# Optimization experiments

Hardware: AMD Instinct MI355X
Metric: run time of the kernel (lower is better)

Reference implementation:

```python
import jax, jax.numpy as jnp
import numpy as np

N = 50000      # nodes
E = 400000     # edges (avg degree 8)
C = 128        # dim_single (node_dim)
DP = 64        # dim_pair (edge_dim)
HID = 256      # dim_egnn_hidden
DEPTH = 4      # depth_equivariant
M_IN = 2 * C + DP  # node_mlp / coord_mlp input dim = 320


def setup_inputs() -> dict:
    key = jax.random.key(0)
    ks = jax.random.split(key, 12)
    def w(k, shape, fan):
        return jax.random.normal(k, shape, jnp.float32) / np.float32(np.sqrt(fan))
    return {
        'single': jax.random.normal(ks[0], (N, C), jnp.float32),
        'pair': jax.random.normal(ks[1], (1,), jnp.float32),  # unused (se3t/ipa disabled)
        'coords': jax.random.normal(ks[2], (N, 3), jnp.float32),
        'edge_index': jax.random.randint(ks[3], (2, E), 0, N, jnp.int32),
        'edge_dist': jax.random.uniform(ks[4], (E,), jnp.float32),
        # stacked per-layer EGNN params (leading DEPTH axis, consumed by lax.scan)
        'We1': w(ks[5], (DEPTH, 1, DP), 1), 'be1': jnp.zeros((DEPTH, DP), jnp.float32),
        'We2': w(ks[6], (DEPTH, DP, DP), DP), 'be2': jnp.zeros((DEPTH, DP), jnp.float32),
        'Wn1': w(ks[7], (DEPTH, M_IN, HID), M_IN), 'bn1': jnp.zeros((DEPTH, HID), jnp.float32),
        'Wn2': w(ks[8], (DEPTH, HID, C), HID), 'bn2': jnp.zeros((DEPTH, C), jnp.float32),
        'Wc1': w(ks[9], (DEPTH, M_IN, HID), M_IN), 'bc1': jnp.zeros((DEPTH, HID), jnp.float32),
        'Wc2': w(ks[10], (DEPTH, HID, 1), HID),  # coord_mlp final layer has no bias
        'gamma': jnp.ones((C,), jnp.float32), 'beta': jnp.zeros((C,), jnp.float32),
    }


def _egnn_stack(h, x, edge_index, edge_dist, params):
    src, dst = edge_index[0], edge_index[1]
    n_nodes = h.shape[0]
    def layer(carry, p):
        h, x = carry
        We1, be1, We2, be2, Wn1, bn1, Wn2, bn2, Wc1, bc1, Wc2 = p
        # edge_mlp(edge_dist)
        ea = jax.nn.silu(edge_dist[:, None] @ We1 + be1) @ We2 + be2        # [E, DP]
        # gather -> concat -> MLP (message)
        mi = jnp.concatenate([h[src], h[dst], ea], axis=-1)                 # [E, 2C+DP]
        m = jax.nn.silu(mi @ Wn1 + bn1) @ Wn2 + bn2                         # [E, C]
        h = h + jax.ops.segment_sum(m, dst, num_segments=n_nodes)          # index_add on dst
        # coordinate update
        cw = jax.nn.silu(mi @ Wc1 + bc1) @ Wc2                              # [E, 1]
        x = x + jax.ops.segment_sum(cw * (x[src] - x[dst]), dst, num_segments=n_nodes)
        return (h, x), None
    (h, x), _ = jax.lax.scan(layer, (h, x), params)
    return h, x


def reference(single, pair, coords, edge_index, edge_dist,
              We1, be1, We2, be2, Wn1, bn1, Wn2, bn2, Wc1, bc1, Wc2,
              gamma, beta):
    h, x = _egnn_stack(single, coords, edge_index, edge_dist,
                       (We1, be1, We2, be2, Wn1, bn1, Wn2, bn2, Wc1, bc1, Wc2))
    # final LayerNorm (eps=1e-5, matching nn.LayerNorm default)
    mu = h.mean(-1, keepdims=True)
    var = ((h - mu) ** 2).mean(-1, keepdims=True)
    out = gamma * (h - mu) * jax.lax.rsqrt(var + 1e-5) + beta
    return out, x
```

## Files before the change

kernel.cpp:

```cpp
#include <hip/hip_runtime.h>
#include <hip/hip_bf16.h>
#include <math.h>

#define NN 50000
#define NE 400000
#define CD 128
#define EPB 64
#define HBINS 50176

typedef __attribute__((ext_vector_type(8))) short bf16x8;
typedef __attribute__((ext_vector_type(4))) float f32x4;

__device__ __forceinline__ float silu_f(float z) {
    return z * __builtin_amdgcn_rcpf(1.f + __expf(-z));
}
__device__ __forceinline__ unsigned short f2bf(float x) {
    unsigned int u = __float_as_uint(x);
    u = (u + 0x7FFFu + ((u >> 16) & 1u)) >> 16;
    return (unsigned short)u;
}
__device__ __forceinline__ unsigned pk_bf16(float a, float b) {
    union { __hip_bfloat162 h2; unsigned u; } cv;
    cv.h2 = __float22bfloat162_rn(make_float2(a, b));
    return cv.u;
}

__global__ __launch_bounds__(256) void hist_kernel(
        const int* __restrict__ dst, int* __restrict__ hist)
{
    int e = blockIdx.x * 256 + threadIdx.x;
    if (e < NE) atomicAdd(&hist[dst[e]], 1);
}

__global__ __launch_bounds__(256) void scan1_kernel(
        const int* __restrict__ hist, int* __restrict__ offs, int* __restrict__ bsum)
{
    __shared__ int sh[256];
    const int t = threadIdx.x;
    const int i = blockIdx.x * 256 + t;
    int v = hist[i];
    sh[t] = v;
    __syncthreads();
    for (int off = 1; off < 256; off <<= 1) {
        int x = (t >= off) ? sh[t - off] : 0;
        __syncthreads();
        sh[t] += x;
        __syncthreads();
    }
    offs[i] = sh[t] - v;
    if (t == 255) bsum[blockIdx.x] = sh[t];
}

__global__ __launch_bounds__(256) void scan2_kernel(int* __restrict__ bsum)
{
    __shared__ int sh[256];
    const int t = threadIdx.x;
    int v = (t < 196) ? bsum[t] : 0;
    sh[t] = v;
    __syncthreads();
    for (int off = 1; off < 256; off <<= 1) {
        int x = (t >= off) ? sh[t - off] : 0;
        __syncthreads();
        sh[t] += x;
        __syncthreads();
    }
    if (t < 196) bsum[t] = sh[t] - v;
}

__global__ __launch_bounds__(256) void scan3_kernel(
        const int* __restrict__ offs, const int* __restrict__ bsum,
        int* __restrict__ cursor)
{
    const int i = blockIdx.x * 256 + threadIdx.x;
    cursor[i] = offs[i] + bsum[blockIdx.x];
}

__global__ __launch_bounds__(256) void scatter_kernel(
        const int* __restrict__ eidx, const float* __restrict__ edist,
        int* __restrict__ cursor,
        int* __restrict__ ssrc, int* __restrict__ sdst, float* __restrict__ sdist)
{
    int e = blockIdx.x * 256 + threadIdx.x;
    if (e < NE) {
        int d = eidx[NE + e];
        int p = atomicAdd(&cursor[d], 1);
        ssrc[p] = eidx[e];
        sdst[p] = d;
        sdist[p] = edist[e];
    }
}

__global__ __launch_bounds__(64) void wbig_prep(
        const float* __restrict__ We2, const float* __restrict__ Wn1,
        const float* __restrict__ Wc1, unsigned short* __restrict__ wbig)
{
    const int l = blockIdx.y;
    const int ntile = blockIdx.x / 10;
    const int ks = blockIdx.x % 10;
    const int lane = threadIdx.x;
    const int n = ntile * 16 + (lane & 15);
    const int kbase = ks * 32 + (lane >> 4) * 8;
    const float* Wn1l = Wn1 + (size_t)l * 320 * 256;
    const float* Wc1l = Wc1 + (size_t)l * 320 * 256;
    const float* We2l = We2 + (size_t)l * 64 * 64;
    const float* W1 = (n < 256) ? Wn1l : Wc1l;
    const int nn = n & 255;
    unsigned short* outp = wbig + ((((size_t)l * 32 + ntile) * 10 + ks) * 64 + lane) * 8;
    #pragma unroll
    for (int j = 0; j < 8; ++j) {
        int k = kbase + j;
        float val;
        if (k < 256) {
            val = W1[(size_t)k * 256 + nn];
        } else {
            int i = k - 256;
            float acc = 0.f;
            #pragma unroll 8
            for (int jj = 0; jj < 64; ++jj)
                acc += We2l[i * 64 + jj] * W1[(size_t)(256 + jj) * 256 + nn];
            val = acc;
        }
        outp[j] = f2bf(val);
    }
}

__global__ __launch_bounds__(64) void wn2_prep(
        const float* __restrict__ Wn2, unsigned short* __restrict__ wn2s)
{
    const int l = blockIdx.y;
    const int ntile = blockIdx.x / 8;
    const int ks = blockIdx.x % 8;
    const int lane = threadIdx.x;
    const int n = ntile * 16 + (lane & 15);
    const int kbase = ks * 32 + (lane >> 4) * 8;
    const float* Wn2l = Wn2 + (size_t)l * 256 * 128;
    unsigned short* outp = wn2s + ((((size_t)l * 8 + ntile) * 8 + ks) * 64 + lane) * 8;
    #pragma unroll
    for (int j = 0; j < 8; ++j)
        outp[j] = f2bf(Wn2l[(size_t)(kbase + j) * 128 + n]);
}

__global__ __launch_bounds__(512) void cep_prep(
        const float* __restrict__ be2,
        const float* __restrict__ Wn1, const float* __restrict__ Wc1,
        const float* __restrict__ bn1, const float* __restrict__ bc1,
        float* __restrict__ cep)
{
    const int l = blockIdx.x;
    const int j = threadIdx.x;
    const int jj = j & 255;
    const float* W1 = ((j < 256) ? Wn1 : Wc1) + (size_t)l * 320 * 256;
    const float* be2l = be2 + l * 64;
    float acc = (j < 256) ? bn1[l * 256 + jj] : bc1[l * 256 + jj];
    #pragma unroll 8
    for (int k = 0; k < 64; ++k)
        acc += be2l[k] * W1[(size_t)(256 + k) * 256 + jj];
    cep[l * 512 + j] = acc;
}

__global__ __launch_bounds__(256) void conv_kernel(
        const float* __restrict__ h, unsigned short* __restrict__ hbf)
{
    const int i = (blockIdx.x * 256 + threadIdx.x) * 4;
    float4 v = *(const float4*)(h + i);
    *(uint2*)(hbf + i) = make_uint2(pk_bf16(v.x, v.y), pk_bf16(v.z, v.w));
}

__global__ __launch_bounds__(512, 4) void edge_kernel(
        const int* __restrict__ ssrc, const int* __restrict__ sdst,
        const float* __restrict__ sdist,
        const float* __restrict__ We1l, const float* __restrict__ be1l,
        const unsigned short* __restrict__ hbf,
        const unsigned short* __restrict__ wbig_l,
        const float* __restrict__ cep_l,
        const float* __restrict__ Wc2l,
        const float* __restrict__ x_in,
        float* __restrict__ Tbar, float* __restrict__ x_out)
{
    __shared__ __align__(16) unsigned short s_A[EPB][328];
    __shared__ __align__(16) unsigned short s_tT[256][72];
    __shared__ __align__(16) float s_cw[EPB][4];
    __shared__ __align__(16) unsigned short s_rid[EPB];
    __shared__ int s_src[EPB], s_dst[EPB];
    __shared__ int s_rdst[EPB];
    __shared__ unsigned long long s_mask;

    const int tid = threadIdx.x;
    const int eb = blockIdx.x * EPB;

    if (tid < EPB) {
        int dv = sdst[eb + tid];
        s_src[tid] = ssrc[eb + tid];
        s_dst[tid] = dv;
        int nxt = (tid == EPB - 1) ? -1 : sdst[eb + tid + 1];
        unsigned long long mk = __ballot(dv != nxt);
        int rid = __popcll(mk & ((1ull << tid) - 1ull));
        s_rid[tid] = (unsigned short)rid;
        if (dv != nxt) s_rdst[rid] = dv;
        if (tid == 0) s_mask = mk;
    }
    {
        const int e = tid >> 3;
        const int j0 = (tid & 7) * 8;
        const float d = sdist[eb + e];
        unsigned tmp[4];
        #pragma unroll
        for (int j = 0; j < 4; ++j) {
            float a = silu_f(d * We1l[j0 + 2 * j] + be1l[j0 + 2 * j]);
            float b = silu_f(d * We1l[j0 + 2 * j + 1] + be1l[j0 + 2 * j + 1]);
            tmp[j] = pk_bf16(a, b);
        }
        *(bf16x8*)&s_A[e][j0 + 256] = *(const bf16x8*)tmp;
    }
    __syncthreads();

    #pragma unroll
    for (int it = 0; it < 4; ++it) {
        const int c = tid + it * 512;
        const int row = c >> 5, ch = c & 31;
        const int node = (ch < 16) ? s_src[row] : s_dst[row];
        const int koff = (ch & 15) * 8;
        bf16x8 v = *(const bf16x8*)(hbf + (size_t)node * CD + koff);
        *(bf16x8*)&s_A[row][ch * 8] = v;
    }
    __syncthreads();

    const int wave = tid >> 6, lane = tid & 63;
    const int m = lane & 15, q = lane >> 4;

    f32x4 acc[4][4];
    #pragma unroll
    for (int nt = 0; nt < 4; ++nt)
        #pragma unroll
        for (int mt = 0; mt < 4; ++mt)
            acc[nt][mt] = (f32x4){0.f, 0.f, 0.f, 0.f};

    __builtin_amdgcn_s_setprio(1);
    if (wave < 4) {
        #pragma unroll
        for (int ks = 0; ks < 10; ++ks) {
            const int koff = ks * 32 + q * 8;
            bf16x8 ef[4];
            #pragma unroll
            for (int mt = 0; mt < 4; ++mt)
                ef[mt] = *(const bf16x8*)&s_A[mt * 16 + m][koff];
            #pragma unroll
            for (int nt = 0; nt < 4; ++nt) {
                bf16x8 wf = *(const bf16x8*)(wbig_l +
                    ((size_t)((wave * 4 + nt) * 10 + ks) * 64 + lane) * 8);
                #pragma unroll
                for (int mt = 0; mt < 4; ++mt)
                    acc[nt][mt] = __builtin_amdgcn_mfma_f32_16x16x32_bf16(
                        ef[mt], wf, acc[nt][mt], 0, 0, 0);
            }
        }
    } else {
        #pragma unroll
        for (int ks = 0; ks < 10; ++ks) {
            const int koff = ks * 32 + q * 8;
            bf16x8 ef[4];
            #pragma unroll
            for (int mt = 0; mt < 4; ++mt)
                ef[mt] = *(const bf16x8*)&s_A[mt * 16 + m][koff];
            #pragma unroll
            for (int nt = 0; nt < 4; ++nt) {
                bf16x8 wf = *(const bf16x8*)(wbig_l +
                    ((size_t)((wave * 4 + nt) * 10 + ks) * 64 + lane) * 8);
                #pragma unroll
                for (int mt = 0; mt < 4; ++mt)
                    acc[nt][mt] = __builtin_amdgcn_mfma_f32_16x16x32_bf16(
                        wf, ef[mt], acc[nt][mt], 0, 0, 0);
            }
        }
    }
    __builtin_amdgcn_s_setprio(0);

    if (wave < 4) {
        #pragma unroll
        for (int nt = 0; nt < 4; ++nt) {
            const int col = (wave * 4 + nt) * 16 + m;
            const float ce = cep_l[col];
            #pragma unroll
            for (int mt = 0; mt < 4; ++mt) {
                float t0 = silu_f(acc[nt][mt][0] + ce);
                float t1 = silu_f(acc[nt][mt][1] + ce);
                float t2 = silu_f(acc[nt][mt][2] + ce);
                float t3 = silu_f(acc[nt][mt][3] + ce);
                *(uint2*)&s_tT[col][(mt * 16 + q * 4) ^ ((m & 3) << 3)] =
                    make_uint2(pk_bf16(t0, t1), pk_bf16(t2, t3));
            }
        }
    } else {
        float p[4] = {0.f, 0.f, 0.f, 0.f};
        #pragma unroll
        for (int nt = 0; nt < 4; ++nt) {
            const int c0 = (wave * 4 + nt) * 16 + q * 4;
            const float4 ce = *(const float4*)&cep_l[c0];
            const float4 wv = *(const float4*)&Wc2l[c0 - 256];
            #pragma unroll
            for (int mt = 0; mt < 4; ++mt) {
                p[mt] += silu_f(acc[nt][mt][0] + ce.x) * wv.x;
                p[mt] += silu_f(acc[nt][mt][1] + ce.y) * wv.y;
                p[mt] += silu_f(acc[nt][mt][2] + ce.z) * wv.z;
                p[mt] += silu_f(acc[nt][mt][3] + ce.w) * wv.w;
            }
        }
        #pragma unroll
        for (int mt = 0; mt < 4; ++mt) {
            p[mt] += __shfl_xor(p[mt], 16);
            p[mt] += __shfl_xor(p[mt], 32);
        }
        if (lane < 16) {
            #pragma unroll
            for (int mt = 0; mt < 4; ++mt)
                s_cw[mt * 16 + lane][wave - 4] = p[mt];
        }
    }
    __syncthreads();

    {
        const unsigned long long mask = s_mask;
        const int nruns = __popcll(mask);
        f32x4 a2[2][4];
        #pragma unroll
        for (int mt2 = 0; mt2 < 2; ++mt2)
            #pragma unroll
            for (int nt = 0; nt < 4; ++nt)
                a2[mt2][nt] = (f32x4){0.f, 0.f, 0.f, 0.f};
        #pragma unroll
        for (int ks = 0; ks < 2; ++ks) {
            bf16x8 af[2];
            #pragma unroll
            for (int mt2 = 0; mt2 < 2; ++mt2)
                af[mt2] = *(const bf16x8*)&s_tT[(wave * 2 + mt2) * 16 + m]
                                           [(ks * 32 + q * 8) ^ ((m & 3) << 3)];
            const unsigned* rp = (const unsigned*)&s_rid[ks * 32 + q * 8];
            const unsigned r01 = rp[0], r23 = rp[1], r45 = rp[2], r67 = rp[3];
            #pragma unroll
            for (int nt = 0; nt < 4; ++nt) {
                const unsigned n = (unsigned)(nt * 16 + m);
                unsigned gw[4];
                gw[0] = ((r01 & 0xFFFFu) == n ? 0x3F80u : 0u) |
                        ((r01 >> 16)      == n ? 0x3F800000u : 0u);
                gw[1] = ((r23 & 0xFFFFu) == n ? 0x3F80u : 0u) |
                        ((r23 >> 16)      == n ? 0x3F800000u : 0u);
                gw[2] = ((r45 & 0xFFFFu) == n ? 0x3F80u : 0u) |
                        ((r45 >> 16)      == n ? 0x3F800000u : 0u);
                gw[3] = ((r67 & 0xFFFFu) == n ? 0x3F80u : 0u) |
                        ((r67 >> 16)      == n ? 0x3F800000u : 0u);
                const bf16x8 bfr = *(const bf16x8*)gw;
                #pragma unroll
                for (int mt2 = 0; mt2 < 2; ++mt2)
                    a2[mt2][nt] = __builtin_amdgcn_mfma_f32_16x16x32_bf16(
                        af[mt2], bfr, a2[mt2][nt], 0, 0, 0);
            }
        }
        #pragma unroll
        for (int nt = 0; nt < 4; ++nt) {
            const int r = nt * 16 + m;
            if (r < nruns) {
                float* bp = Tbar + (size_t)s_rdst[r] * 256;
                const bool bdry = (r == 0) || (r == nruns - 1);
                #pragma unroll
                for (int mt2 = 0; mt2 < 2; ++mt2) {
                    const int c = (wave * 2 + mt2) * 16 + q * 4;
                    if (bdry) {
                        atomicAdd(&bp[c],     a2[mt2][nt][0]);
                        atomicAdd(&bp[c + 1], a2[mt2][nt][1]);
                        atomicAdd(&bp[c + 2], a2[mt2][nt][2]);
                        atomicAdd(&bp[c + 3], a2[mt2][nt][3]);
                    } else {
                        *(f32x4*)&bp[c] = a2[mt2][nt];
                    }
                }
            }
        }
    }
    if (wave == 2) {
        const int e = lane;
        float4 pv = *(const float4*)&s_cw[e][0];
        float cw = pv.x + pv.y + pv.z + pv.w;
        int sn = s_src[e], dn = s_dst[e];
        float dx0 = x_in[sn * 3 + 0] - x_in[dn * 3 + 0];
        float dx1 = x_in[sn * 3 + 1] - x_in[dn * 3 + 1];
        float dx2 = x_in[sn * 3 + 2] - x_in[dn * 3 + 2];
        atomicAdd(&x_out[dn * 3 + 0], cw * dx0);
        atomicAdd(&x_out[dn * 3 + 1], cw * dx1);
        atomicAdd(&x_out[dn * 3 + 2], cw * dx2);
    }
}

__global__ __launch_bounds__(256) void node_kernel(
        const float* __restrict__ Tbar, const int* __restrict__ deg,
        const unsigned short* __restrict__ wn2_l, const float* __restrict__ bn2l,
        float* __restrict__ h, unsigned short* __restrict__ hbf)
{
    const int nb = blockIdx.x * 64;
    const int tid = threadIdx.x;
    const int wave = tid >> 6, lane = tid & 63;
    const int m = lane & 15, q = lane >> 4;

    f32x4 acc[2][4];
    #pragma unroll
    for (int nt = 0; nt < 2; ++nt)
        #pragma unroll
        for (int mt = 0; mt < 4; ++mt)
            acc[nt][mt] = (f32x4){0.f, 0.f, 0.f, 0.f};

    #pragma unroll
    for (int ks = 0; ks < 8; ++ks) {
        bf16x8 af[4];
        #pragma unroll
        for (int mt = 0; mt < 4; ++mt) {
            const int node = nb + mt * 16 + m;
            if (node < NN) {
                const float* tp = Tbar + (size_t)node * 256 + ks * 32 + q * 8;
                float4 f0 = *(const float4*)tp;
                float4 f1 = *(const float4*)(tp + 4);
                unsigned u[4] = { pk_bf16(f0.x, f0.y), pk_bf16(f0.z, f0.w),
                                  pk_bf16(f1.x, f1.y), pk_bf16(f1.z, f1.w) };
                af[mt] = *(const bf16x8*)u;
            } else {
                af[mt] = (bf16x8){0,0,0,0,0,0,0,0};
            }
        }
        #pragma unroll
        for (int nt = 0; nt < 2; ++nt) {
            bf16x8 wf = *(const bf16x8*)(wn2_l +
                ((size_t)((wave * 2 + nt) * 8 + ks) * 64 + lane) * 8);
            #pragma unroll
            for (int mt = 0; mt < 4; ++mt)
                acc[nt][mt] = __builtin_amdgcn_mfma_f32_16x16x32_bf16(af[mt], wf, acc[nt][mt], 0, 0, 0);
        }
    }

    {
        float* tz = (float*)Tbar;
        #pragma unroll
        for (int ks = 0; ks < 8; ++ks) {
            #pragma unroll
            for (int mt = 0; mt < 4; ++mt) {
                const int node = nb + mt * 16 + m;
                if (node < NN && wave == (ks & 3)) {
                    float* tp = tz + (size_t)node * 256 + ks * 32 + q * 8;
                    *(f32x4*)tp       = (f32x4){0.f, 0.f, 0.f, 0.f};
                    *(f32x4*)(tp + 4) = (f32x4){0.f, 0.f, 0.f, 0.f};
                }
            }
        }
    }

    #pragma unroll
    for (int nt = 0; nt < 2; ++nt) {
        const int col = (wave * 2 + nt) * 16 + m;
        const float bb = bn2l[col];
        #pragma unroll
        for (int mt = 0; mt < 4; ++mt) {
            #pragma unroll
            for (int i = 0; i < 4; ++i) {
                const int node = nb + mt * 16 + q * 4 + i;
                if (node < NN) {
                    float val = acc[nt][mt][i] + (float)deg[node] * bb
                              + h[(size_t)node * CD + col];
                    h[(size_t)node * CD + col] = val;
                    hbf[(size_t)node * CD + col] = f2bf(val);
                }
            }
        }
    }
}

__global__ __launch_bounds__(256) void final_kernel(
        const float* __restrict__ h, const float* __restrict__ x,
        const float* __restrict__ gamma, const float* __restrict__ beta,
        float* __restrict__ out)
{
    const int lane = threadIdx.x & 63;
    const int wave = threadIdx.x >> 6;
    const int n = blockIdx.x * 4 + wave;
    float v0 = h[(size_t)n * CD + lane];
    float v1 = h[(size_t)n * CD + 64 + lane];
    float ssum = v0 + v1;
    for (int off = 32; off; off >>= 1) ssum += __shfl_xor(ssum, off);
    float mu = ssum * (1.f / 128.f);
    float d0 = v0 - mu, d1 = v1 - mu;
    float sq = d0 * d0 + d1 * d1;
    for (int off = 32; off; off >>= 1) sq += __shfl_xor(sq, off);
    float rstd = rsqrtf(sq * (1.f / 128.f) + 1e-5f);
    out[(size_t)n * CD + lane]      = gamma[lane]      * d0 * rstd + beta[lane];
    out[(size_t)n * CD + 64 + lane] = gamma[64 + lane] * d1 * rstd + beta[64 + lane];
    if (threadIdx.x < 12) {
        int nn = blockIdx.x * 4 + threadIdx.x / 3;
        int c = threadIdx.x % 3;
        out[(size_t)NN * CD + nn * 3 + c] = x[nn * 3 + c];
    }
}

static inline size_t align_up(size_t v) { return (v + 255) & ~(size_t)255; }

extern "C" void kernel_launch(void* const* d_in, const int* in_sizes, int n_in,
                              void* d_out, int out_size, void* d_ws, size_t ws_size,
                              hipStream_t stream)
{
    const float* single = (const float*)d_in[0];
    const float* coords = (const float*)d_in[2];
    const int*   eidx   = (const int*)d_in[3];
    const float* edist  = (const float*)d_in[4];
    const float* We1 = (const float*)d_in[5];
    const float* be1 = (const float*)d_in[6];
    const float* We2 = (const float*)d_in[7];
    const float* be2 = (const float*)d_in[8];
    const float* Wn1 = (const float*)d_in[9];
    const float* bn1 = (const float*)d_in[10];
    const float* Wn2 = (const float*)d_in[11];
    const float* bn2 = (const float*)d_in[12];
    const float* Wc1 = (const float*)d_in[13];
    const float* bc1 = (const float*)d_in[14];
    const float* Wc2 = (const float*)d_in[15];
    const float* gamma = (const float*)d_in[16];
    const float* beta  = (const float*)d_in[17];
    float* out = (float*)d_out;

    char* w = (char*)d_ws;
    float* h0  = (float*)w;  w += align_up((size_t)NN * CD * 4);
    float* x0  = (float*)w;  w += align_up((size_t)NN * 3 * 4);
    float* x1  = (float*)w;  w += align_up((size_t)NN * 3 * 4);
    unsigned short* hbf  = (unsigned short*)w; w += align_up((size_t)NN * CD * 2);
    unsigned short* wbig = (unsigned short*)w; w += align_up((size_t)4 * 512 * 320 * 2);
    unsigned short* wn2s = (unsigned short*)w; w += align_up((size_t)4 * 256 * 128 * 2);
    float* cep = (float*)w;  w += align_up((size_t)4 * 512 * 4);
    int* hist   = (int*)w;   w += align_up((size_t)HBINS * 4);
    int* offs   = (int*)w;   w += align_up((size_t)HBINS * 4);
    int* cursor = (int*)w;   w += align_up((size_t)HBINS * 4);
    int* bsum   = (int*)w;   w += align_up((size_t)256 * 4);
    int* ssrc   = (int*)w;   w += align_up((size_t)NE * 4);
    int* sdst   = (int*)w;   w += align_up((size_t)NE * 4);
    float* sdist = (float*)w; w += align_up((size_t)NE * 4);
    float* Tbar = (float*)w; w += align_up((size_t)NN * 256 * 4);

    hipMemsetAsync(hist, 0, (size_t)HBINS * 4, stream);
    hist_kernel<<<(NE + 255) / 256, 256, 0, stream>>>(eidx + NE, hist);
    scan1_kernel<<<HBINS / 256, 256, 0, stream>>>(hist, offs, bsum);
    scan2_kernel<<<1, 256, 0, stream>>>(bsum);
    scan3_kernel<<<HBINS / 256, 256, 0, stream>>>(offs, bsum, cursor);
    scatter_kernel<<<(NE + 255) / 256, 256, 0, stream>>>(eidx, edist, cursor, ssrc, sdst, sdist);

    wbig_prep<<<dim3(320, 4), 64, 0, stream>>>(We2, Wn1, Wc1, wbig);
    wn2_prep<<<dim3(64, 4), 64, 0, stream>>>(Wn2, wn2s);
    cep_prep<<<4, 512, 0, stream>>>(be2, Wn1, Wc1, bn1, bc1, cep);

    hipMemcpyAsync(h0, single, (size_t)NN * CD * 4, hipMemcpyDeviceToDevice, stream);
    hipMemcpyAsync(x0, coords, (size_t)NN * 3 * 4, hipMemcpyDeviceToDevice, stream);
    conv_kernel<<<(NN * CD) / 1024, 256, 0, stream>>>(single, hbf);

    hipMemsetAsync(Tbar, 0, (size_t)NN * 256 * 4, stream);

    float* xc = x0; float* xn = x1;
    for (int l = 0; l < 4; ++l) {
        hipMemcpyAsync(xn, xc, (size_t)NN * 3 * 4, hipMemcpyDeviceToDevice, stream);
        edge_kernel<<<NE / EPB, 512, 0, stream>>>(
            ssrc, sdst, sdist,
            We1 + l * 64, be1 + l * 64,
            hbf,
            wbig + (size_t)l * 512 * 320,
            cep + l * 512,
            Wc2 + l * 256,
            xc, Tbar, xn);
        node_kernel<<<(NN + 63) / 64, 256, 0, stream>>>(
            Tbar, hist,
            wn2s + (size_t)l * 256 * 128,
            bn2 + l * CD, h0, hbf);
        float* t = xc; xc = xn; xn = t;
    }
    final_kernel<<<NN / 4, 256, 0, stream>>>(h0, xc, gamma, beta, out);
}
```

Before: 1.410 ms.

## Store interior per-node aggregates in bf16, keep fp32 atomics only for boundary nodes

The edge kernel writes aggregated per-node hidden activations for runs fully inside a block as bf16 into a separate buffer. Runs on block boundaries still use fp32 atomics into a side buffer. A per-node flag tells the node kernel which buffer to read. This halves traffic for most aggregate writes and reads, and replaces the zeroing loop in the node kernel with a bf16 memset plus a small zeroing kernel that clears only boundary rows. It also drops the setprio hints around the MFMA loops. Nodes with no edges read the memset zero bf16 buffer. The cost is extra launches per layer and a flag lookup in the node kernel.

```diff
diff --git a/kernel.cpp b/kernel.cpp
--- a/kernel.cpp
+++ b/kernel.cpp
@@ -6,6 +6,7 @@
 #define NE 400000
 #define CD 128
 #define EPB 64
+#define NBLK (NE / EPB)
 #define HBINS 50176
 
 typedef __attribute__((ext_vector_type(8))) short bf16x8;
@@ -88,6 +89,26 @@
         sdst[p] = d;
         sdist[p] = edist[e];
     }
+}
+
+__global__ __launch_bounds__(256) void bflag_kernel(
+        const int* __restrict__ sdst, unsigned char* __restrict__ bflag)
+{
+    int b = blockIdx.x * 256 + threadIdx.x;
+    if (b < NBLK) {
+        bflag[sdst[b * EPB]] = 1;
+        bflag[sdst[b * EPB + EPB - 1]] = 1;
+    }
+}
+
+__global__ __launch_bounds__(128) void zside_kernel(
+        const int* __restrict__ sdst, float* __restrict__ Tf32)
+{
+    const int b = blockIdx.x;
+    const int t = threadIdx.x;
+    const int r = (t < 64) ? sdst[b * EPB] : sdst[b * EPB + EPB - 1];
+    *(float4*)(Tf32 + (size_t)r * 256 + (t & 63) * 4) =
+        make_float4(0.f, 0.f, 0.f, 0.f);
 }
 
 __global__ __launch_bounds__(64) void wbig_prep(
@@ -175,7 +196,8 @@
         const float* __restrict__ cep_l,
         const float* __restrict__ Wc2l,
         const float* __restrict__ x_in,
-        float* __restrict__ Tbar, float* __restrict__ x_out)
+        unsigned short* __restrict__ Tbf, float* __restrict__ Tf32,
+        float* __restrict__ x_out)
 {
     __shared__ __align__(16) unsigned short s_A[EPB][328];
     __shared__ __align__(16) unsigned short s_tT[256][72];
@@ -235,7 +257,6 @@
         for (int mt = 0; mt < 4; ++mt)
             acc[nt][mt] = (f32x4){0.f, 0.f, 0.f, 0.f};
 
-    __builtin_amdgcn_s_setprio(1);
     if (wave < 4) {
         #pragma unroll
         for (int ks = 0; ks < 10; ++ks) {
@@ -273,7 +294,6 @@
             }
         }
     }
-    __builtin_amdgcn_s_setprio(0);
 
     if (wave < 4) {
         #pragma unroll
@@ -359,18 +379,25 @@
         for (int nt = 0; nt < 4; ++nt) {
             const int r = nt * 16 + m;
             if (r < nruns) {
-                float* bp = Tbar + (size_t)s_rdst[r] * 256;
                 const bool bdry = (r == 0) || (r == nruns - 1);
-                #pragma unroll
-                for (int mt2 = 0; mt2 < 2; ++mt2) {
-                    const int c = (wave * 2 + mt2) * 16 + q * 4;
-                    if (bdry) {
+                if (bdry) {
+                    float* bp = Tf32 + (size_t)s_rdst[r] * 256;
+                    #pragma unroll
+                    for (int mt2 = 0; mt2 < 2; ++mt2) {
+                        const int c = (wave * 2 + mt2) * 16 + q * 4;
                         atomicAdd(&bp[c],     a2[mt2][nt][0]);
                         atomicAdd(&bp[c + 1], a2[mt2][nt][1]);
                         atomicAdd(&bp[c + 2], a2[mt2][nt][2]);
                         atomicAdd(&bp[c + 3], a2[mt2][nt][3]);
-                    } else {
-                        *(f32x4*)&bp[c] = a2[mt2][nt];
+                    }
+                } else {
+                    unsigned short* bp = Tbf + (size_t)s_rdst[r] * 256;
+                    #pragma unroll
+                    for (int mt2 = 0; mt2 < 2; ++mt2) {
+                        const int c = (wave * 2 + mt2) * 16 + q * 4;
+                        *(uint2*)&bp[c] = make_uint2(
+                            pk_bf16(a2[mt2][nt][0], a2[mt2][nt][1]),
+                            pk_bf16(a2[mt2][nt][2], a2[mt2][nt][3]));
                     }
                 }
             }
@@ -391,7 +418,8 @@
 }
 
 __global__ __launch_bounds__(256) void node_kernel(
-        const float* __restrict__ Tbar, const int* __restrict__ deg,
+        const unsigned short* __restrict__ Tbf, const float* __restrict__ Tf32,
+        const unsigned char* __restrict__ bflag, const int* __restrict__ deg,
         const unsigned short* __restrict__ wn2_l, const float* __restrict__ bn2l,
         float* __restrict__ h, unsigned short* __restrict__ hbf)
 {
@@ -400,6 +428,13 @@
     const int wave = tid >> 6, lane = tid & 63;
     const int m = lane & 15, q = lane >> 4;
 
+    int fl[4];
+    #pragma unroll
+    for (int mt = 0; mt < 4; ++mt) {
+        const int node = nb + mt * 16 + m;
+        fl[mt] = (node < NN) ? (int)bflag[node] : 0;
+    }
+
     f32x4 acc[2][4];
     #pragma unroll
     for (int nt = 0; nt < 2; ++nt)
@@ -414,12 +449,16 @@
         for (int mt = 0; mt < 4; ++mt) {
             const int node = nb + mt * 16 + m;
             if (node < NN) {
-                const float* tp = Tbar + (size_t)node * 256 + ks * 32 + q * 8;
-                float4 f0 = *(const float4*)tp;
-                float4 f1 = *(const float4*)(tp + 4);
-                unsigned u[4] = { pk_bf16(f0.x, f0.y), pk_bf16(f0.z, f0.w),
-                                  pk_bf16(f1.x, f1.y), pk_bf16(f1.z, f1.w) };
-                af[mt] = *(const bf16x8*)u;
+                if (!fl[mt]) {
+                    af[mt] = *(const bf16x8*)(Tbf + (size_t)node * 256 + ks * 32 + q * 8);
+                } else {
+                    const float* tp = Tf32 + (size_t)node * 256 + ks * 32 + q * 8;
+                    float4 f0 = *(const float4*)tp;
+                    float4 f1 = *(const float4*)(tp + 4);
+                    unsigned u[4] = { pk_bf16(f0.x, f0.y), pk_bf16(f0.z, f0.w),
+                                      pk_bf16(f1.x, f1.y), pk_bf16(f1.z, f1.w) };
+                    af[mt] = *(const bf16x8*)u;
+                }
             } else {
                 af[mt] = (bf16x8){0,0,0,0,0,0,0,0};
             }
@@ -433,23 +472,6 @@
                 acc[nt][mt] = __builtin_amdgcn_mfma_f32_16x16x32_bf16(af[mt], wf, acc[nt][mt], 0, 0, 0);
         }
     }
-
-    {
-        float* tz = (float*)Tbar;
-        #pragma unroll
-        for (int ks = 0; ks < 8; ++ks) {
-            #pragma unroll
-            for (int mt = 0; mt < 4; ++mt) {
-                const int node = nb + mt * 16 + m;
-                if (node < NN && wave == (ks & 3)) {
-                    float* tp = tz + (size_t)node * 256 + ks * 32 + q * 8;
-                    *(f32x4*)tp       = (f32x4){0.f, 0.f, 0.f, 0.f};
-                    *(f32x4*)(tp + 4) = (f32x4){0.f, 0.f, 0.f, 0.f};
-                }
-            }
-        }
-    }
-
     #pragma unroll
     for (int nt = 0; nt < 2; ++nt) {
         const int col = (wave * 2 + nt) * 16 + m;
@@ -536,7 +558,9 @@
     int* ssrc   = (int*)w;   w += align_up((size_t)NE * 4);
     int* sdst   = (int*)w;   w += align_up((size_t)NE * 4);
     float* sdist = (float*)w; w += align_up((size_t)NE * 4);
-    float* Tbar = (float*)w; w += align_up((size_t)NN * 256 * 4);
+    unsigned char* bflag = (unsigned char*)w; w += align_up((size_t)NN);
+    unsigned short* Tbf = (unsigned short*)w; w += align_up((size_t)NN * 256 * 2);
+    float* Tf32 = (float*)w; w += align_up((size_t)NN * 256 * 4);
 
     hipMemsetAsync(hist, 0, (size_t)HBINS * 4, stream);
     hist_kernel<<<(NE + 255) / 256, 256, 0, stream>>>(eidx + NE, hist);
@@ -544,6 +568,8 @@
     scan2_kernel<<<1, 256, 0, stream>>>(bsum);
     scan3_kernel<<<HBINS / 256, 256, 0, stream>>>(offs, bsum, cursor);
     scatter_kernel<<<(NE + 255) / 256, 256, 0, stream>>>(eidx, edist, cursor, ssrc, sdst, sdist);
+    hipMemsetAsync(bflag, 0, (size_t)NN, stream);
+    bflag_kernel<<<(NBLK + 255) / 256, 256, 0, stream>>>(sdst, bflag);
 
     wbig_prep<<<dim3(320, 4), 64, 0, stream>>>(We2, Wn1, Wc1, wbig);
     wn2_prep<<<dim3(64, 4), 64, 0, stream>>>(Wn2, wn2s);
@@ -553,21 +579,21 @@
     hipMemcpyAsync(x0, coords, (size_t)NN * 3 * 4, hipMemcpyDeviceToDevice, stream);
     conv_kernel<<<(NN * CD) / 1024, 256, 0, stream>>>(single, hbf);
 
-    hipMemsetAsync(Tbar, 0, (size_t)NN * 256 * 4, stream);
-
     float* xc = x0; float* xn = x1;
     for (int l = 0; l < 4; ++l) {
+        hipMemsetAsync(Tbf, 0, (size_t)NN * 256 * 2, stream);
+        zside_kernel<<<NBLK, 128, 0, stream>>>(sdst, Tf32);
         hipMemcpyAsync(xn, xc, (size_t)NN * 3 * 4, hipMemcpyDeviceToDevice, stream);
-        edge_kernel<<<NE / EPB, 512, 0, stream>>>(
+        edge_kernel<<<NBLK, 512, 0, stream>>>(
             ssrc, sdst, sdist,
             We1 + l * 64, be1 + l * 64,
             hbf,
             wbig + (size_t)l * 512 * 320,
             cep + l * 512,
             Wc2 + l * 256,
-            xc, Tbar, xn);
+            xc, Tbf, Tf32, xn);
         node_kernel<<<(NN + 63) / 64, 256, 0, stream>>>(
-            Tbar, hist,
+            Tbf, Tf32, bflag, hist,
             wn2s + (size_t)l * 256 * 128,
             bn2 + l * CD, h0, hbf);
         float* t = xc; xc = xn; xn = t;
```

New measurement: 1.356 ms. 1.04x faster.
